# Performance work log

Hardware: AMD Instinct MI355X
Metric: run time of the kernel (lower is better)

Reference implementation:

```python
import jax, jax.numpy as jnp
import numpy as np

FEAT = 1024
B = 1024
S = 64


def setup_inputs() -> dict:
    key = jax.random.key(0)
    ks = jax.random.split(key, 6)
    scale_ih = 1.0 / np.sqrt(2 * FEAT)
    scale_hh = 1.0 / np.sqrt(FEAT)
    return {
        "query": jax.random.normal(ks[0], (B, FEAT), jnp.float32) * 0.1,
        "support_context": jax.random.normal(ks[1], (S, FEAT), jnp.float32) * 0.1,
        "W_ih": jax.random.normal(ks[2], (4 * FEAT, 2 * FEAT), jnp.float32) * scale_ih,
        "W_hh": jax.random.normal(ks[3], (4 * FEAT, FEAT), jnp.float32) * scale_hh,
        "b_ih": jax.random.normal(ks[4], (4 * FEAT,), jnp.float32) * scale_hh,
        "b_hh": jax.random.normal(ks[5], (4 * FEAT,), jnp.float32) * scale_hh,
    }


def reference(query, support_context, W_ih, W_hh, b_ih, b_hh):
    # query: [B, F]; support_context: [S, F]; steps == S
    hidden = query
    cell = jnp.zeros_like(query)
    support_t = support_context.T  # [F, S]

    def step(carry, _):
        h, c = carry
        attn = jax.nn.softmax(h @ support_t, axis=1)          # [B, S]
        readout = attn @ support_context                      # [B, F]
        x = jnp.concatenate([query, readout], axis=1)         # [B, 2F]
        gates = x @ W_ih.T + b_ih + h @ W_hh.T + b_hh          # [B, 4F]
        i, f, g, o = jnp.split(gates, 4, axis=1)               # torch LSTMCell gate order
        c_new = jax.nn.sigmoid(f) * c + jax.nn.sigmoid(i) * jnp.tanh(g)
        h_new = jax.nn.sigmoid(o) * jnp.tanh(c_new) + query   # skip connection per original
        return (h_new, c_new), None

    (hidden, cell), _ = jax.lax.scan(step, (hidden, cell), None,
                                     length=support_context.shape[0])
    return hidden
```

## Files before the change

### kernel.cpp

```cpp
#include <hip/hip_runtime.h>
#include <hip/hip_bf16.h>


typedef __attribute__((ext_vector_type(8))) __bf16 bf16x8;
typedef __attribute__((ext_vector_type(4))) float f32x4;
typedef __attribute__((ext_vector_type(8))) unsigned short ushort8;

__device__ __forceinline__ ushort f2bf(float f) {
  union { float f; unsigned int u; } v; v.f = f;
  unsigned int u = v.u;
  u += 0x7FFFu + ((u >> 16) & 1u);
  return (ushort)(u >> 16);
}
__device__ __forceinline__ float bf2f(ushort u) {
  union { float f; unsigned int u; } v; v.u = ((unsigned int)u) << 16; return v.f;
}
__device__ __forceinline__ float sigm_(float x) { return 1.f / (1.f + __expf(-x)); }
__device__ __forceinline__ float tanh_(float x) {
  x = fminf(15.f, fmaxf(-15.f, x));
  float e = __expf(2.f * x);
  return (e - 1.f) / (e + 1.f);
}
__device__ __forceinline__ void async16(ushort* lds, const ushort* g) {
  __builtin_amdgcn_global_load_lds(
      (const __attribute__((address_space(1))) void*)g,
      (__attribute__((address_space(3))) void*)lds, 16, 0, 0);
}
__device__ __forceinline__ int permrow(int n) {
  int g = n >> 10, j = n & 1023;
  return ((j >> 4) << 6) | (g << 4) | (j & 15);
}

__global__ __launch_bounds__(256) void prep_kernel(
    const float* __restrict__ query, const float* __restrict__ support,
    const float* __restrict__ W_ih, const float* __restrict__ W_hh,
    const float* __restrict__ b_ih, const float* __restrict__ b_hh,
    ushort* __restrict__ Wq_bf, ushort* __restrict__ Wcomb,
    float* __restrict__ bias_p, ushort* __restrict__ X0,
    float* __restrict__ c, ushort* __restrict__ Wr_bf,
    ushort* __restrict__ Sb)
{
  int g = blockIdx.x * 256 + threadIdx.x;
  int n = g >> 10, k = g & 1023;
  int np = permrow(n);
  Wq_bf[(size_t)np * 1024 + k] = f2bf(W_ih[(size_t)n * 2048 + k]);
  Wr_bf[(size_t)n * 1024 + k]  = f2bf(W_ih[(size_t)n * 2048 + 1024 + k]);
  Wcomb[(size_t)np * 1088 + k] = f2bf(W_hh[(size_t)n * 1024 + k]);
  if (g < 1024 * 1024) {
    X0[g] = f2bf(query[g]);
    c[g] = 0.f;
  }
  if (g < 4096) bias_p[permrow(g)] = b_ih[g] + b_hh[g];
  if (g < 65536) Sb[g] = f2bf(support[g]);
}

__global__ __launch_bounds__(256) void sw_mfma(
    const ushort* __restrict__ Wr, const ushort* __restrict__ Sb,
    ushort* __restrict__ Wcomb)
{
  __shared__ ushort As[3][128 * 32];
  __shared__ ushort Bs[3][64 * 32];
  const int t = threadIdx.x;
  const int bm0 = blockIdx.x * 128;
  const int w = t >> 6, l = t & 63;
  const int wm = w * 32;
  const int srow = t >> 2, scol = (t & 3) * 8;
  const ushort* ga0 = Wr + (size_t)(bm0 + srow) * 1024 + scol;
  const ushort* ga1 = Wr + (size_t)(bm0 + 64 + srow) * 1024 + scol;
  const ushort* gb0 = Sb + (size_t)srow * 1024 + scol;
  const int fr = l & 15, fk = (l >> 4) * 8, fq = l >> 4;
  f32x4 acc[2][4] = {};
  const int nt = 32;
  async16(&As[0][t * 8], ga0); async16(&As[0][2048 + t * 8], ga1);
  async16(&Bs[0][t * 8], gb0);
  async16(&As[1][t * 8], ga0 + 32); async16(&As[1][2048 + t * 8], ga1 + 32);
  async16(&Bs[1][t * 8], gb0 + 32);
  for (int it = 0; it < nt; it++) {
    if (it + 1 < nt) { asm volatile("s_waitcnt vmcnt(3)" ::: "memory"); }
    else             { asm volatile("s_waitcnt vmcnt(0)" ::: "memory"); }
    __builtin_amdgcn_s_barrier();
    __builtin_amdgcn_sched_barrier(0);
    const int b = it % 3;
    const ushort* pa = &As[b][(wm + fr) * 32 + fk];
    const ushort* pb = &Bs[b][fr * 32 + fk];
    bf16x8 af[2], bfv[4];
#pragma unroll
    for (int mi = 0; mi < 2; mi++) af[mi] = *(const bf16x8*)(pa + mi * 512);
#pragma unroll
    for (int ni = 0; ni < 4; ni++) bfv[ni] = *(const bf16x8*)(pb + ni * 512);
    if (it + 2 < nt) {
      const int pbuf = (it + 2) % 3;
      const int k0 = (it + 2) << 5;
      async16(&As[pbuf][t * 8], ga0 + k0); async16(&As[pbuf][2048 + t * 8], ga1 + k0);
      async16(&Bs[pbuf][t * 8], gb0 + k0);
    }
#pragma unroll
    for (int mi = 0; mi < 2; mi++)
#pragma unroll
      for (int ni = 0; ni < 4; ni++)
        acc[mi][ni] = __builtin_amdgcn_mfma_f32_16x16x32_bf16(af[mi], bfv[ni], acc[mi][ni], 0, 0, 0);
  }
#pragma unroll
  for (int mi = 0; mi < 2; mi++)
#pragma unroll
    for (int ni = 0; ni < 4; ni++) {
      int s = ni * 16 + fr;
      int row0 = bm0 + wm + mi * 16 + fq * 4;
#pragma unroll
      for (int jj = 0; jj < 4; jj++)
        Wcomb[(size_t)permrow(row0 + jj) * 1088 + 1024 + s] = f2bf(acc[mi][ni][jj]);
    }
}

__global__ __launch_bounds__(256) void gemm_base(
    const ushort* __restrict__ A, const ushort* __restrict__ Bw,
    const float* __restrict__ bias, float* __restrict__ Cout)
{
  __shared__ ushort As[3][2][64 * 32];
  __shared__ ushort Bs[3][2][128 * 32];
  const int t = threadIdx.x;
  const int bid = blockIdx.x;
  const int xcd = bid & 7, idx = bid >> 3;
  const int bx = idx & 15, byy = idx >> 4;
  const int by = xcd * 4 + byy;
  const int m0 = bx * 64, n0 = by * 128;
  const int w = t >> 6, l = t & 63;
  const int wm = (w >> 1) * 32, wn = (w & 1) * 64;
  const int srow = t >> 2, scol = (t & 3) * 8;
  const ushort* ga  = A  + (size_t)(m0 + srow) * 1024 + scol;
  const ushort* gb0 = Bw + (size_t)(n0 + srow) * 1024 + scol;
  const ushort* gb1 = Bw + (size_t)(n0 + 64 + srow) * 1024 + scol;
  const int fr = l & 15, fk = (l >> 4) * 8, fq = l >> 4;
  f32x4 acc[2][4] = {};
  const int nt = 16;
#define BSTAGE(buf, k0)                                       \
  async16(&As[buf][0][t * 8], ga + (k0));                     \
  async16(&As[buf][1][t * 8], ga + (k0) + 32);                \
  async16(&Bs[buf][0][t * 8], gb0 + (k0));                    \
  async16(&Bs[buf][0][2048 + t * 8], gb1 + (k0));             \
  async16(&Bs[buf][1][t * 8], gb0 + (k0) + 32);               \
  async16(&Bs[buf][1][2048 + t * 8], gb1 + (k0) + 32);
  BSTAGE(0, 0)
  BSTAGE(1, 64)
  for (int it = 0; it < nt; it++) {
    if (it + 1 < nt) { asm volatile("s_waitcnt vmcnt(6)" ::: "memory"); }
    else             { asm volatile("s_waitcnt vmcnt(0)" ::: "memory"); }
    __builtin_amdgcn_s_barrier();
    __builtin_amdgcn_sched_barrier(0);
    if (it + 2 < nt) { const int pb = (it + 2) % 3; const int k0 = (it + 2) << 6; BSTAGE(pb, k0) }
    const int b = it % 3;
#pragma unroll
    for (int kk = 0; kk < 2; kk++) {
      const ushort* pa = &As[b][kk][(wm + fr) * 32 + fk];
      const ushort* pb2 = &Bs[b][kk][(wn + fr) * 32 + fk];
      bf16x8 af[2], bfv[4];
#pragma unroll
      for (int mi = 0; mi < 2; mi++) af[mi] = *(const bf16x8*)(pa + mi * 512);
#pragma unroll
      for (int ni = 0; ni < 4; ni++) bfv[ni] = *(const bf16x8*)(pb2 + ni * 512);
      __builtin_amdgcn_s_setprio(1);
#pragma unroll
      for (int mi = 0; mi < 2; mi++)
#pragma unroll
        for (int ni = 0; ni < 4; ni++)
          acc[mi][ni] = __builtin_amdgcn_mfma_f32_16x16x32_bf16(af[mi], bfv[ni], acc[mi][ni], 0, 0, 0);
      __builtin_amdgcn_s_setprio(0);
    }
  }
#undef BSTAGE
#pragma unroll
  for (int mi = 0; mi < 2; mi++)
#pragma unroll
    for (int ni = 0; ni < 4; ni++) {
      int col = n0 + wn + ni * 16 + fr;
      int row0 = m0 + wm + mi * 16 + fq * 4;
      float bv = bias[col];
#pragma unroll
      for (int jj = 0; jj < 4; jj++)
        Cout[(size_t)(row0 + jj) * 4096 + col] = acc[mi][ni][jj] + bv;
    }
}

__global__ __launch_bounds__(256, 3) void gemm_fused(
    const ushort* __restrict__ A,
    const ushort* __restrict__ Wcomb,
    const ushort* __restrict__ Sb,
    const float* __restrict__ base,
    float* __restrict__ cbuf, const float* __restrict__ query,
    ushort* __restrict__ Xout, float* __restrict__ outp)
{
  __shared__ ushort As[2][2][64 * 32];
  __shared__ ushort Bs[2][2][128 * 32];
  const int t = threadIdx.x;
  const int bid = blockIdx.x;
  const int xcd = bid & 7, idx = bid >> 3;
  const int bx = idx & 15, byy = idx >> 4;
  const int by = xcd * 4 + byy;
  const int m0 = bx * 64, n0 = by * 128;
  const int w = t >> 6, l = t & 63;
  const int wm = (w >> 1) * 32, wn = (w & 1) * 64;
  const int srow = t >> 2, scol = (t & 3) * 8;
  const ushort* ga  = A + (size_t)(m0 + srow) * 1024 + scol;
  const ushort* gb0 = Wcomb + (size_t)(n0 + srow) * 1088 + scol;
  const ushort* gb1 = Wcomb + (size_t)(n0 + 64 + srow) * 1088 + scol;
  const int fr = l & 15, fk = (l >> 4) * 8, fq = l >> 4;
  const ushort* gsb = Sb + (size_t)((w & 1) * 32 + fr) * 1024 + fk;
  f32x4 acc[2][4] = {};
  f32x4 lacc[2][2] = {};
#define FSTAGE_A(buf, k0)                                     \
  async16(&As[buf][0][t * 8], ga + (k0));                     \
  async16(&As[buf][1][t * 8], ga + (k0) + 32);
#define FSTAGE_B(buf, k0)                                     \
  async16(&Bs[buf][0][t * 8], gb0 + (k0));                    \
  async16(&Bs[buf][0][2048 + t * 8], gb1 + (k0));             \
  async16(&Bs[buf][1][t * 8], gb0 + (k0) + 32);               \
  async16(&Bs[buf][1][2048 + t * 8], gb1 + (k0) + 32);
  FSTAGE_A(0, 0) FSTAGE_B(0, 0)
  asm volatile("s_waitcnt vmcnt(0)" ::: "memory");
  for (int it = 0; it < 16; it++) {
    __builtin_amdgcn_s_barrier();
    const int cur = it & 1, nxt = cur ^ 1;
    const int k0 = it << 6;
    const int ka = (it < 15) ? (k0 + 64) : 960;
    const int kb = (it < 15) ? (k0 + 64) : 1024;
    FSTAGE_A(nxt, ka) FSTAGE_B(nxt, kb)
    bf16x8 sb00 = *(const bf16x8*)(gsb + k0);
    bf16x8 sb01 = *(const bf16x8*)(gsb + k0 + 32);
    bf16x8 sb10 = *(const bf16x8*)(gsb + k0 + 16384);
    bf16x8 sb11 = *(const bf16x8*)(gsb + k0 + 16384 + 32);
    bf16x8 af2[2][2];
#pragma unroll
    for (int kk = 0; kk < 2; kk++) {
      const ushort* pa = &As[cur][kk][(wm + fr) * 32 + fk];
      const ushort* pb2 = &Bs[cur][kk][(wn + fr) * 32 + fk];
      bf16x8 bfv[4];
#pragma unroll
      for (int mi = 0; mi < 2; mi++) af2[kk][mi] = *(const bf16x8*)(pa + mi * 512);
#pragma unroll
      for (int ni = 0; ni < 4; ni++) bfv[ni] = *(const bf16x8*)(pb2 + ni * 512);
      __builtin_amdgcn_s_setprio(1);
#pragma unroll
      for (int mi = 0; mi < 2; mi++)
#pragma unroll
        for (int ni = 0; ni < 4; ni++)
          acc[mi][ni] = __builtin_amdgcn_mfma_f32_16x16x32_bf16(af2[kk][mi], bfv[ni], acc[mi][ni], 0, 0, 0);
      __builtin_amdgcn_s_setprio(0);
    }
    asm volatile("s_waitcnt vmcnt(6)" ::: "memory");
    __builtin_amdgcn_sched_barrier(0);
    lacc[0][0] = __builtin_amdgcn_mfma_f32_16x16x32_bf16(af2[0][0], sb00, lacc[0][0], 0, 0, 0);
    lacc[0][1] = __builtin_amdgcn_mfma_f32_16x16x32_bf16(af2[0][0], sb10, lacc[0][1], 0, 0, 0);
    lacc[1][0] = __builtin_amdgcn_mfma_f32_16x16x32_bf16(af2[0][1], sb00, lacc[1][0], 0, 0, 0);
    lacc[1][1] = __builtin_amdgcn_mfma_f32_16x16x32_bf16(af2[0][1], sb10, lacc[1][1], 0, 0, 0);
    lacc[0][0] = __builtin_amdgcn_mfma_f32_16x16x32_bf16(af2[1][0], sb01, lacc[0][0], 0, 0, 0);
    lacc[0][1] = __builtin_amdgcn_mfma_f32_16x16x32_bf16(af2[1][0], sb11, lacc[0][1], 0, 0, 0);
    lacc[1][0] = __builtin_amdgcn_mfma_f32_16x16x32_bf16(af2[1][1], sb01, lacc[1][0], 0, 0, 0);
    lacc[1][1] = __builtin_amdgcn_mfma_f32_16x16x32_bf16(af2[1][1], sb11, lacc[1][1], 0, 0, 0);
    asm volatile("s_waitcnt vmcnt(0)" ::: "memory");
  }
#undef FSTAGE_A
#undef FSTAGE_B
  __builtin_amdgcn_s_barrier();
  {
    float* lg = (float*)&Bs[1][0][0];
    const int sbase = (w & 1) * 32;
#pragma unroll
    for (int mi = 0; mi < 2; mi++)
#pragma unroll
      for (int ni = 0; ni < 2; ni++) {
        int s = sbase + ni * 16 + fr;
        int r0 = wm + mi * 16 + fq * 4;
#pragma unroll
        for (int jj = 0; jj < 4; jj++)
          lg[(r0 + jj) * 64 + s] = lacc[mi][ni][jj];
      }
  }
  __syncthreads();
  {
    const int r = t >> 2, q = t & 3;
    float* lg = (float*)&Bs[1][0][0];
    float p[16];
#pragma unroll
    for (int i = 0; i < 16; i++) p[i] = lg[r * 64 + q * 16 + i];
    float mx = p[0];
#pragma unroll
    for (int i = 1; i < 16; i++) mx = fmaxf(mx, p[i]);
    mx = fmaxf(mx, __shfl_xor(mx, 1));
    mx = fmaxf(mx, __shfl_xor(mx, 2));
    float sm = 0.f;
#pragma unroll
    for (int i = 0; i < 16; i++) { p[i] = __expf(p[i] - mx); sm += p[i]; }
    sm += __shfl_xor(sm, 1);
    sm += __shfl_xor(sm, 2);
    float inv = 1.f / sm;
    ushort* at = &As[0][q >> 1][r * 32 + (q & 1) * 16];
#pragma unroll
    for (int i = 0; i < 16; i++) at[i] = f2bf(p[i] * inv);
  }
  __syncthreads();
#pragma unroll
  for (int kk = 0; kk < 2; kk++) {
    const ushort* pa = &As[0][kk][(wm + fr) * 32 + fk];
    const ushort* pb2 = &Bs[0][kk][(wn + fr) * 32 + fk];
    bf16x8 af[2], bfv[4];
#pragma unroll
    for (int mi = 0; mi < 2; mi++) af[mi] = *(const bf16x8*)(pa + mi * 512);
#pragma unroll
    for (int ni = 0; ni < 4; ni++) bfv[ni] = *(const bf16x8*)(pb2 + ni * 512);
    __builtin_amdgcn_s_setprio(1);
#pragma unroll
    for (int mi = 0; mi < 2; mi++)
#pragma unroll
      for (int ni = 0; ni < 4; ni++)
        acc[mi][ni] = __builtin_amdgcn_mfma_f32_16x16x32_bf16(af[mi], bfv[ni], acc[mi][ni], 0, 0, 0);
    __builtin_amdgcn_s_setprio(0);
  }
  const int jcol = (((n0 + wn) >> 6) << 4) + fr;
#pragma unroll
  for (int mi = 0; mi < 2; mi++) {
#pragma unroll
    for (int jj = 0; jj < 4; jj++) {
      int row = m0 + wm + mi * 16 + fq * 4 + jj;
      const float* bp = base + (size_t)row * 4096 + (n0 + wn);
      float gi = acc[mi][0][jj] + bp[fr];
      float gf = acc[mi][1][jj] + bp[16 + fr];
      float gg = acc[mi][2][jj] + bp[32 + fr];
      float go = acc[mi][3][jj] + bp[48 + fr];
      size_t cidx = (size_t)row * 1024 + jcol;
      float cv = cbuf[cidx];
      float cn = sigm_(gf) * cv + sigm_(gi) * tanh_(gg);
      float hn = sigm_(go) * tanh_(cn) + query[cidx];
      cbuf[cidx] = cn;
      Xout[cidx] = f2bf(hn);
      if (outp) outp[cidx] = hn;
    }
  }
}

extern "C" void kernel_launch(void* const* d_in, const int* in_sizes, int n_in,
                              void* d_out, int out_size, void* d_ws, size_t ws_size,
                              hipStream_t stream) {
  const float* query   = (const float*)d_in[0];
  const float* support = (const float*)d_in[1];
  const float* W_ih    = (const float*)d_in[2];
  const float* W_hh    = (const float*)d_in[3];
  const float* b_ih    = (const float*)d_in[4];
  const float* b_hh    = (const float*)d_in[5];
  float* out = (float*)d_out;

  char* ws = (char*)d_ws;
  size_t off = 0;
  auto alloc = [&](size_t bytes) {
    void* p = ws + off;
    off += (bytes + 255) & ~(size_t)255;
    return p;
  };
  ushort* Wq_bf  = (ushort*)alloc((size_t)4096 * 1024 * 2);
  ushort* Wcomb  = (ushort*)alloc((size_t)4096 * 1088 * 2);
  ushort* Wr_bf  = (ushort*)alloc((size_t)4096 * 1024 * 2);
  ushort* Sb     = (ushort*)alloc((size_t)64 * 1024 * 2);
  float*  bias_p = (float*) alloc((size_t)4096 * 4);
  float*  base   = (float*) alloc((size_t)1024 * 4096 * 4);
  ushort* X0     = (ushort*)alloc((size_t)1024 * 1024 * 2);
  ushort* X1     = (ushort*)alloc((size_t)1024 * 1024 * 2);
  float*  c      = (float*) alloc((size_t)1024 * 1024 * 4);

  prep_kernel<<<16384, 256, 0, stream>>>(query, support, W_ih, W_hh, b_ih, b_hh,
                                         Wq_bf, Wcomb, bias_p, X0, c, Wr_bf, Sb);
  sw_mfma<<<32, 256, 0, stream>>>(Wr_bf, Sb, Wcomb);
  gemm_base<<<512, 256, 0, stream>>>(X0, Wq_bf, bias_p, base);
  for (int step = 0; step < 64; step++) {
    ushort* Xc = (step & 1) ? X1 : X0;
    ushort* Xn = (step & 1) ? X0 : X1;
    gemm_fused<<<512, 256, 0, stream>>>(Xc, Wcomb, Sb, base,
                                        c, query, Xn,
                                        (step == 63) ? out : nullptr);
  }
}
```

Before: 1.956 ms.

## Load fused-GEMM operands directly from global memory instead of LDS staging

```diff
diff --git a/kernel.cpp b/kernel.cpp
--- a/kernel.cpp
+++ b/kernel.cpp
@@ -4,16 +4,14 @@
 
 typedef __attribute__((ext_vector_type(8))) __bf16 bf16x8;
 typedef __attribute__((ext_vector_type(4))) float f32x4;
-typedef __attribute__((ext_vector_type(8))) unsigned short ushort8;
+
+#define MFMA __builtin_amdgcn_mfma_f32_16x16x32_bf16
 
 __device__ __forceinline__ ushort f2bf(float f) {
   union { float f; unsigned int u; } v; v.f = f;
   unsigned int u = v.u;
   u += 0x7FFFu + ((u >> 16) & 1u);
   return (ushort)(u >> 16);
-}
-__device__ __forceinline__ float bf2f(ushort u) {
-  union { float f; unsigned int u; } v; v.u = ((unsigned int)u) << 16; return v.f;
 }
 __device__ __forceinline__ float sigm_(float x) { return 1.f / (1.f + __expf(-x)); }
 __device__ __forceinline__ float tanh_(float x) {
@@ -98,7 +96,7 @@
     for (int mi = 0; mi < 2; mi++)
 #pragma unroll
       for (int ni = 0; ni < 4; ni++)
-        acc[mi][ni] = __builtin_amdgcn_mfma_f32_16x16x32_bf16(af[mi], bfv[ni], acc[mi][ni], 0, 0, 0);
+        acc[mi][ni] = MFMA(af[mi], bfv[ni], acc[mi][ni], 0, 0, 0);
   }
 #pragma unroll
   for (int mi = 0; mi < 2; mi++)
@@ -163,7 +161,7 @@
       for (int mi = 0; mi < 2; mi++)
 #pragma unroll
         for (int ni = 0; ni < 4; ni++)
-          acc[mi][ni] = __builtin_amdgcn_mfma_f32_16x16x32_bf16(af[mi], bfv[ni], acc[mi][ni], 0, 0, 0);
+          acc[mi][ni] = MFMA(af[mi], bfv[ni], acc[mi][ni], 0, 0, 0);
       __builtin_amdgcn_s_setprio(0);
     }
   }
@@ -189,8 +187,8 @@
     float* __restrict__ cbuf, const float* __restrict__ query,
     ushort* __restrict__ Xout, float* __restrict__ outp)
 {
-  __shared__ ushort As[2][2][64 * 32];
-  __shared__ ushort Bs[2][2][128 * 32];
+  __shared__ float  lg[64 * 65];
+  __shared__ ushort at[64 * 72];
   const int t = threadIdx.x;
   const int bid = blockIdx.x;
   const int xcd = bid & 7, idx = bid >> 3;
@@ -199,70 +197,45 @@
   const int m0 = bx * 64, n0 = by * 128;
   const int w = t >> 6, l = t & 63;
   const int wm = (w >> 1) * 32, wn = (w & 1) * 64;
-  const int srow = t >> 2, scol = (t & 3) * 8;
-  const ushort* ga  = A + (size_t)(m0 + srow) * 1024 + scol;
-  const ushort* gb0 = Wcomb + (size_t)(n0 + srow) * 1088 + scol;
-  const ushort* gb1 = Wcomb + (size_t)(n0 + 64 + srow) * 1088 + scol;
   const int fr = l & 15, fk = (l >> 4) * 8, fq = l >> 4;
-  const ushort* gsb = Sb + (size_t)((w & 1) * 32 + fr) * 1024 + fk;
+  const ushort* pa0 = A + (size_t)(m0 + wm + fr) * 1024 + fk;
+  const ushort* pa1 = pa0 + 16 * 1024;
+  const ushort* pbm0 = Wcomb + (size_t)(n0 + wn + fr) * 1088 + fk;
+  const ushort* pbm1 = pbm0 + 16 * 1088;
+  const ushort* pbm2 = pbm0 + 32 * 1088;
+  const ushort* pbm3 = pbm0 + 48 * 1088;
+  const ushort* gsb0 = Sb + (size_t)((w & 1) * 32 + fr) * 1024 + fk;
+  const ushort* gsb1 = gsb0 + 16 * 1024;
   f32x4 acc[2][4] = {};
   f32x4 lacc[2][2] = {};
-#define FSTAGE_A(buf, k0)                                     \
-  async16(&As[buf][0][t * 8], ga + (k0));                     \
-  async16(&As[buf][1][t * 8], ga + (k0) + 32);
-#define FSTAGE_B(buf, k0)                                     \
-  async16(&Bs[buf][0][t * 8], gb0 + (k0));                    \
-  async16(&Bs[buf][0][2048 + t * 8], gb1 + (k0));             \
-  async16(&Bs[buf][1][t * 8], gb0 + (k0) + 32);               \
-  async16(&Bs[buf][1][2048 + t * 8], gb1 + (k0) + 32);
-  FSTAGE_A(0, 0) FSTAGE_B(0, 0)
-  asm volatile("s_waitcnt vmcnt(0)" ::: "memory");
-  for (int it = 0; it < 16; it++) {
-    __builtin_amdgcn_s_barrier();
-    const int cur = it & 1, nxt = cur ^ 1;
-    const int k0 = it << 6;
-    const int ka = (it < 15) ? (k0 + 64) : 960;
-    const int kb = (it < 15) ? (k0 + 64) : 1024;
-    FSTAGE_A(nxt, ka) FSTAGE_B(nxt, kb)
-    bf16x8 sb00 = *(const bf16x8*)(gsb + k0);
-    bf16x8 sb01 = *(const bf16x8*)(gsb + k0 + 32);
-    bf16x8 sb10 = *(const bf16x8*)(gsb + k0 + 16384);
-    bf16x8 sb11 = *(const bf16x8*)(gsb + k0 + 16384 + 32);
-    bf16x8 af2[2][2];
-#pragma unroll
-    for (int kk = 0; kk < 2; kk++) {
-      const ushort* pa = &As[cur][kk][(wm + fr) * 32 + fk];
-      const ushort* pb2 = &Bs[cur][kk][(wn + fr) * 32 + fk];
-      bf16x8 bfv[4];
-#pragma unroll
-      for (int mi = 0; mi < 2; mi++) af2[kk][mi] = *(const bf16x8*)(pa + mi * 512);
-#pragma unroll
-      for (int ni = 0; ni < 4; ni++) bfv[ni] = *(const bf16x8*)(pb2 + ni * 512);
-      __builtin_amdgcn_s_setprio(1);
-#pragma unroll
-      for (int mi = 0; mi < 2; mi++)
-#pragma unroll
-        for (int ni = 0; ni < 4; ni++)
-          acc[mi][ni] = __builtin_amdgcn_mfma_f32_16x16x32_bf16(af2[kk][mi], bfv[ni], acc[mi][ni], 0, 0, 0);
-      __builtin_amdgcn_s_setprio(0);
-    }
-    asm volatile("s_waitcnt vmcnt(6)" ::: "memory");
-    __builtin_amdgcn_sched_barrier(0);
-    lacc[0][0] = __builtin_amdgcn_mfma_f32_16x16x32_bf16(af2[0][0], sb00, lacc[0][0], 0, 0, 0);
-    lacc[0][1] = __builtin_amdgcn_mfma_f32_16x16x32_bf16(af2[0][0], sb10, lacc[0][1], 0, 0, 0);
-    lacc[1][0] = __builtin_amdgcn_mfma_f32_16x16x32_bf16(af2[0][1], sb00, lacc[1][0], 0, 0, 0);
-    lacc[1][1] = __builtin_amdgcn_mfma_f32_16x16x32_bf16(af2[0][1], sb10, lacc[1][1], 0, 0, 0);
-    lacc[0][0] = __builtin_amdgcn_mfma_f32_16x16x32_bf16(af2[1][0], sb01, lacc[0][0], 0, 0, 0);
-    lacc[0][1] = __builtin_amdgcn_mfma_f32_16x16x32_bf16(af2[1][0], sb11, lacc[0][1], 0, 0, 0);
-    lacc[1][0] = __builtin_amdgcn_mfma_f32_16x16x32_bf16(af2[1][1], sb01, lacc[1][0], 0, 0, 0);
-    lacc[1][1] = __builtin_amdgcn_mfma_f32_16x16x32_bf16(af2[1][1], sb11, lacc[1][1], 0, 0, 0);
-    asm volatile("s_waitcnt vmcnt(0)" ::: "memory");
-  }
-#undef FSTAGE_A
-#undef FSTAGE_B
-  __builtin_amdgcn_s_barrier();
+#pragma unroll
+  for (int it = 0; it < 16; ++it) {
+#pragma unroll
+    for (int kk = 0; kk < 2; ++kk) {
+      const int ko = it * 64 + kk * 32;
+      bf16x8 a0 = *(const bf16x8*)(pa0 + ko);
+      bf16x8 a1 = *(const bf16x8*)(pa1 + ko);
+      bf16x8 s0 = *(const bf16x8*)(gsb0 + ko);
+      bf16x8 s1 = *(const bf16x8*)(gsb1 + ko);
+      bf16x8 b0 = *(const bf16x8*)(pbm0 + ko);
+      bf16x8 b1 = *(const bf16x8*)(pbm1 + ko);
+      bf16x8 b2 = *(const bf16x8*)(pbm2 + ko);
+      bf16x8 b3 = *(const bf16x8*)(pbm3 + ko);
+      acc[0][0] = MFMA(a0, b0, acc[0][0], 0, 0, 0);
+      acc[0][1] = MFMA(a0, b1, acc[0][1], 0, 0, 0);
+      acc[0][2] = MFMA(a0, b2, acc[0][2], 0, 0, 0);
+      acc[0][3] = MFMA(a0, b3, acc[0][3], 0, 0, 0);
+      acc[1][0] = MFMA(a1, b0, acc[1][0], 0, 0, 0);
+      acc[1][1] = MFMA(a1, b1, acc[1][1], 0, 0, 0);
+      acc[1][2] = MFMA(a1, b2, acc[1][2], 0, 0, 0);
+      acc[1][3] = MFMA(a1, b3, acc[1][3], 0, 0, 0);
+      lacc[0][0] = MFMA(a0, s0, lacc[0][0], 0, 0, 0);
+      lacc[0][1] = MFMA(a0, s1, lacc[0][1], 0, 0, 0);
+      lacc[1][0] = MFMA(a1, s0, lacc[1][0], 0, 0, 0);
+      lacc[1][1] = MFMA(a1, s1, lacc[1][1], 0, 0, 0);
+    }
+  }
   {
-    float* lg = (float*)&Bs[1][0][0];
     const int sbase = (w & 1) * 32;
 #pragma unroll
     for (int mi = 0; mi < 2; mi++)
@@ -272,16 +245,15 @@
         int r0 = wm + mi * 16 + fq * 4;
 #pragma unroll
         for (int jj = 0; jj < 4; jj++)
-          lg[(r0 + jj) * 64 + s] = lacc[mi][ni][jj];
+          lg[(r0 + jj) * 65 + s] = lacc[mi][ni][jj];
       }
   }
   __syncthreads();
   {
     const int r = t >> 2, q = t & 3;
-    float* lg = (float*)&Bs[1][0][0];
     float p[16];
 #pragma unroll
-    for (int i = 0; i < 16; i++) p[i] = lg[r * 64 + q * 16 + i];
+    for (int i = 0; i < 16; i++) p[i] = lg[r * 65 + q * 16 + i];
     float mx = p[0];
 #pragma unroll
     for (int i = 1; i < 16; i++) mx = fmaxf(mx, p[i]);
@@ -293,27 +265,29 @@
     sm += __shfl_xor(sm, 1);
     sm += __shfl_xor(sm, 2);
     float inv = 1.f / sm;
-    ushort* at = &As[0][q >> 1][r * 32 + (q & 1) * 16];
-#pragma unroll
-    for (int i = 0; i < 16; i++) at[i] = f2bf(p[i] * inv);
+    ushort* atp = &at[r * 72 + q * 16];
+#pragma unroll
+    for (int i = 0; i < 16; i++) atp[i] = f2bf(p[i] * inv);
   }
   __syncthreads();
 #pragma unroll
-  for (int kk = 0; kk < 2; kk++) {
-    const ushort* pa = &As[0][kk][(wm + fr) * 32 + fk];
-    const ushort* pb2 = &Bs[0][kk][(wn + fr) * 32 + fk];
-    bf16x8 af[2], bfv[4];
-#pragma unroll
-    for (int mi = 0; mi < 2; mi++) af[mi] = *(const bf16x8*)(pa + mi * 512);
-#pragma unroll
-    for (int ni = 0; ni < 4; ni++) bfv[ni] = *(const bf16x8*)(pb2 + ni * 512);
-    __builtin_amdgcn_s_setprio(1);
-#pragma unroll
-    for (int mi = 0; mi < 2; mi++)
-#pragma unroll
-      for (int ni = 0; ni < 4; ni++)
-        acc[mi][ni] = __builtin_amdgcn_mfma_f32_16x16x32_bf16(af[mi], bfv[ni], acc[mi][ni], 0, 0, 0);
-    __builtin_amdgcn_s_setprio(0);
+  for (int kk = 0; kk < 2; ++kk) {
+    const int ko = 1024 + kk * 32;
+    const int ka = kk * 32;
+    bf16x8 a0 = *(const bf16x8*)&at[(wm + fr) * 72 + ka + fk];
+    bf16x8 a1 = *(const bf16x8*)&at[(wm + 16 + fr) * 72 + ka + fk];
+    bf16x8 b0 = *(const bf16x8*)(pbm0 + ko);
+    bf16x8 b1 = *(const bf16x8*)(pbm1 + ko);
+    bf16x8 b2 = *(const bf16x8*)(pbm2 + ko);
+    bf16x8 b3 = *(const bf16x8*)(pbm3 + ko);
+    acc[0][0] = MFMA(a0, b0, acc[0][0], 0, 0, 0);
+    acc[0][1] = MFMA(a0, b1, acc[0][1], 0, 0, 0);
+    acc[0][2] = MFMA(a0, b2, acc[0][2], 0, 0, 0);
+    acc[0][3] = MFMA(a0, b3, acc[0][3], 0, 0, 0);
+    acc[1][0] = MFMA(a1, b0, acc[1][0], 0, 0, 0);
+    acc[1][1] = MFMA(a1, b1, acc[1][1], 0, 0, 0);
+    acc[1][2] = MFMA(a1, b2, acc[1][2], 0, 0, 0);
+    acc[1][3] = MFMA(a1, b3, acc[1][3], 0, 0, 0);
   }
   const int jcol = (((n0 + wn) >> 6) << 4) + fr;
 #pragma unroll
```

Measured after the change: 4.413 ms. +125.6%, slower.
